# Kernel tuning notes

Hardware: AMD Instinct MI355X
Metric: run time of the kernel (lower is better)

## Reference

```python
import jax, jax.numpy as jnp
import numpy as np

B, T, D_IN, H, D2, D_OUT, N_CULT = 1024, 128, 32, 512, 256, 16, 32


def setup_inputs() -> dict:
    key = jax.random.key(0)
    ks = jax.random.split(key, 16)
    s = 0.05
    return {
        "input": jax.random.normal(ks[0], (B, T, D_IN), jnp.float32),
        "hn": jnp.zeros((1, B, H), jnp.float32),
        "cultivars": jax.random.randint(ks[1], (B, 1), 0, N_CULT, jnp.int32),
        "W1": jax.random.normal(ks[2], (D2, D_IN), jnp.float32) * s,
        "b1": jnp.zeros((D2,), jnp.float32),
        "W2": jax.random.normal(ks[3], (H, D2), jnp.float32) * s,
        "b2": jnp.zeros((H,), jnp.float32),
        "W_ih": jax.random.normal(ks[4], (3 * H, H), jnp.float32) * s,
        "W_hh": jax.random.normal(ks[5], (3 * H, H), jnp.float32) * s,
        "b_ih": jnp.zeros((3 * H,), jnp.float32),
        "b_hh": jnp.zeros((3 * H,), jnp.float32),
        "W3": jax.random.normal(ks[6], (D2, H), jnp.float32) * s,
        "b3": jnp.zeros((D2,), jnp.float32),
        "Wh": jax.random.normal(ks[7], (N_CULT, D_OUT, D2), jnp.float32) * s,
        "bh": jnp.zeros((N_CULT, D_OUT), jnp.float32),
    }


def _gru(x, h0, W_ih, W_hh, b_ih, b_hh):
    # x: [B,T,H]; h0: [B,H]. PyTorch GRU gate order: r, z, n.
    gx = jnp.einsum('bth,gh->btg', x, W_ih) + b_ih  # [B,T,3H]
    gx = jnp.swapaxes(gx, 0, 1)  # [T,B,3H]

    def step(h, gx_t):
        gh = h @ W_hh.T + b_hh
        xr, xz, xn = jnp.split(gx_t, 3, axis=-1)
        hr, hz, hnn = jnp.split(gh, 3, axis=-1)
        r = jax.nn.sigmoid(xr + hr)
        z = jax.nn.sigmoid(xz + hz)
        n = jnp.tanh(xn + r * hnn)
        h_new = (1.0 - z) * n + z * h
        return h_new, None

    h_last, _ = jax.lax.scan(step, h0, gx)
    return h_last  # [B,H]


def reference(input, hn, cultivars, W1, b1, W2, b2, W_ih, W_hh, b_ih, b_hh, W3, b3, Wh, bh):
    x = input @ W1.T + b1          # [B,T,D2]
    x = x @ W2.T + b2              # [B,T,H]
    h_last = _gru(x, hn[0], W_ih, W_hh, b_ih, b_hh)  # [B,H]
    hn_out = h_last[None]          # [1,B,H]
    out = jax.nn.relu(hn_out)
    out = jax.nn.relu(out @ W3.T + b3)[0]  # [B,D2]
    cult = cultivars[:, 0]
    # grouped per-sample head: params[i] = Wh[cult[i]] @ out[i] + bh[cult[i]]
    params = jnp.einsum('bd,bod->bo', out, Wh[cult]) + bh[cult]  # [B,D_OUT]
    return (params, hn_out)
```

## Files before the change

### kernel.cpp

```cpp
#include <hip/hip_runtime.h>


#define T_STEPS 128
#define PITCH   516
#define SLAB_ROWS 64
#define LDS_BYTES (SLAB_ROWS * PITCH * 2)

typedef __attribute__((ext_vector_type(8))) short short8;
typedef __attribute__((ext_vector_type(4))) float f32x4;
typedef __attribute__((ext_vector_type(4))) float float4v;
typedef unsigned short u16;
typedef unsigned long long u64;

static __device__ __forceinline__ u16 f2bf(float f) {
    unsigned int u = __builtin_bit_cast(unsigned int, f);
    u += 0x7FFFu + ((u >> 16) & 1u);
    return (u16)(u >> 16);
}
static __device__ __forceinline__ f32x4 mfma16(short8 a, short8 b, f32x4 c) {
    return __builtin_amdgcn_mfma_f32_16x16x32_bf16(a, b, c, 0, 0, 0);
}
static __device__ __forceinline__ void st_h16(u16* p, short8 v) {
    struct W { u64 a, b; } w = __builtin_bit_cast(W, v);
    u64* q = (u64*)p;
    __hip_atomic_store(q + 0, w.a, __ATOMIC_RELAXED, __HIP_MEMORY_SCOPE_AGENT);
    __hip_atomic_store(q + 1, w.b, __ATOMIC_RELAXED, __HIP_MEMORY_SCOPE_AGENT);
}
static __device__ __forceinline__ u64 ld_sc1_u64(const u16* p) {
    return __hip_atomic_load((const u64*)p, __ATOMIC_RELAXED, __HIP_MEMORY_SCOPE_AGENT);
}
static __device__ __forceinline__ short8 lds8(const u16* p) {
    u64 lo = *(const u64*)p;
    u64 hi = *(const u64*)(p + 4);
    struct W { u64 a, b; } w{lo, hi};
    return __builtin_bit_cast(short8, w);
}

#define WS_HBUF0 0
#define WS_HBUF1 1048576
#define WS_W21   2097152
#define WS_B21   2162688
#define WS_WEFF  2164736
#define WS_BEFF  2263040
#define WS_FLAGS 2269184

__global__ void k_prep0(const float* __restrict__ W1, const float* __restrict__ b1,
                        const float* __restrict__ W2, const float* __restrict__ b2,
                        float* __restrict__ W21, float* __restrict__ b21,
                        unsigned* __restrict__ flags) {
    if (blockIdx.x == 0) {
        __hip_atomic_store(&flags[threadIdx.x], 0u, __ATOMIC_RELAXED, __HIP_MEMORY_SCOPE_AGENT);
        __hip_atomic_store(&flags[256 + threadIdx.x], 0u, __ATOMIC_RELAXED, __HIP_MEMORY_SCOPE_AGENT);
    }
    int gid = blockIdx.x * 256 + threadIdx.x;
    int k = gid >> 5, d = gid & 31;
    float acc = 0.f;
    for (int j = 0; j < 256; ++j)
        acc += W2[k * 256 + j] * W1[j * 32 + d];
    W21[k * 32 + d] = acc;
    if (d == 0) {
        float bb = b2[k];
        for (int j = 0; j < 256; ++j) bb += W2[k * 256 + j] * b1[j];
        b21[k] = bb;
    }
}

__global__ void k_prep1(const float* __restrict__ W_ih, const float* __restrict__ b_ih,
                        const float* __restrict__ W21, const float* __restrict__ b21,
                        u16* __restrict__ Weff, float* __restrict__ beff) {
    int gid = blockIdx.x * 256 + threadIdx.x;
    int g = gid >> 5, d = gid & 31;
    float acc = 0.f;
    for (int k = 0; k < 512; ++k)
        acc += W_ih[g * 512 + k] * W21[k * 32 + d];
    Weff[g * 32 + d] = f2bf(acc);
    if (d == 0) {
        float bb = b_ih[g];
        for (int k = 0; k < 512; ++k) bb += W_ih[g * 512 + k] * b21[k];
        beff[g] = bb;
    }
}

static __device__ __forceinline__ void bar_arrive(unsigned* gflags, int slot, unsigned v) {
    __syncthreads();
    if (threadIdx.x == 0)
        __hip_atomic_store(&gflags[slot], v, __ATOMIC_RELAXED, __HIP_MEMORY_SCOPE_AGENT);
}
static __device__ __forceinline__ void bar_wait(const unsigned* gflags, unsigned v) {
    if (threadIdx.x < 64) {
        int idx = threadIdx.x & 15;
        for (;;) {
            unsigned f = __hip_atomic_load(&gflags[idx], __ATOMIC_RELAXED, __HIP_MEMORY_SCOPE_AGENT);
            if (__ballot(f >= v) == ~0ull) break;
            __builtin_amdgcn_s_sleep(1);
        }
    }
    __syncthreads();
}

__launch_bounds__(256, 1)
__global__ void k_gru(const float* __restrict__ input, const float* __restrict__ hn,
                      const float* __restrict__ W_hh, const float* __restrict__ b_hh,
                      const u16* __restrict__ Weff, const float* __restrict__ beff,
                      u16* __restrict__ hbuf0, u16* __restrict__ hbuf1,
                      unsigned* __restrict__ flags, float* __restrict__ hn_out) {
    extern __shared__ __align__(16) u16 slab[];

    const int tid  = threadIdx.x;
    const int wave = tid >> 6, lane = tid & 63;
    const int col_l = lane & 15, quad = lane >> 4;
    const int blk = blockIdx.x;
    const int grp = blk & 15, colg = blk >> 4;
    const int colbase = colg * 32;
    const int grpbase = grp * 64;
    const int wcol = wave & 1, wm = wave >> 1;
    const int cb = colbase + wcol * 16;
    unsigned* gflags = flags + grp * 32;

    {
        int b = grpbase + colg * 4 + wave;
        const float* src = hn + (size_t)b * 512 + lane * 8;
        short8 v;
        #pragma unroll
        for (int e = 0; e < 8; ++e) v[e] = (short)f2bf(src[e]);
        st_h16(hbuf0 + (size_t)b * 512 + lane * 8, v);
    }
    short8 whhf[3][16];
    #pragma unroll
    for (int g3 = 0; g3 < 3; ++g3) {
        const float* wrow = W_hh + (size_t)(g3 * 512 + cb + col_l) * 512;
        #pragma unroll
        for (int kc = 0; kc < 16; ++kc) {
            const float* p = wrow + kc * 32 + quad * 8;
            short8 v;
            #pragma unroll
            for (int e = 0; e < 8; ++e) v[e] = (short)f2bf(p[e]);
            whhf[g3][kc] = v;
        }
    }
    short8 bwx[3];
    float bx[3], bhh[3];
    #pragma unroll
    for (int g3 = 0; g3 < 3; ++g3) {
        int nr = g3 * 512 + cb + col_l;
        bwx[g3] = *(const short8*)(Weff + nr * 32 + quad * 8);
        bx[g3]  = beff[nr];
        bhh[g3] = b_hh[nr];
    }
    float hs[2][4];
    #pragma unroll
    for (int m = 0; m < 2; ++m)
        #pragma unroll
        for (int i = 0; i < 4; ++i)
            hs[m][i] = hn[(size_t)(grpbase + (wm * 2 + m) * 16 + quad * 4 + i) * 512 + cb + col_l];

    bar_arrive(gflags, colg, 1u);

    u16* bufs[2] = { hbuf0, hbuf1 };
    #pragma unroll 1
    for (int t = 0; t < T_STEPS; ++t) {
        const u16* hsrc = bufs[t & 1];
        u16* hdst = bufs[(t + 1) & 1];

        float xf[2][8];
        #pragma unroll
        for (int m = 0; m < 2; ++m) {
            const float* xp = input + (size_t)(grpbase + (wm * 2 + m) * 16 + col_l) * 4096 + t * 32 + quad * 8;
            float4v a = *(const float4v*)xp;
            float4v b = *(const float4v*)(xp + 4);
            #pragma unroll
            for (int e = 0; e < 4; ++e) { xf[m][e] = a[e]; xf[m][4 + e] = b[e]; }
        }

        bar_wait(gflags, (unsigned)(t + 1));

        {
            u64 stg[32];
            #pragma unroll
            for (int r16 = 0; r16 < 16; ++r16)
                #pragma unroll
                for (int j = 0; j < 2; ++j)
                    stg[r16 * 2 + j] = ld_sc1_u64(hsrc + (size_t)(grpbase + wave * 16 + r16) * 512 + j * 256 + lane * 4);
            #pragma unroll
            for (int r16 = 0; r16 < 16; ++r16)
                #pragma unroll
                for (int j = 0; j < 2; ++j)
                    *(u64*)&slab[(wave * 16 + r16) * PITCH + j * 256 + lane * 4] = stg[r16 * 2 + j];
        }
        __syncthreads();

        #pragma unroll
        for (int m = 0; m < 2; ++m) {
            short8 ax;
            #pragma unroll
            for (int e = 0; e < 8; ++e) ax[e] = (short)f2bf(xf[m][e]);
            f32x4 z4 = { 0.f, 0.f, 0.f, 0.f };
            f32x4 ar  = mfma16(ax, bwx[0], z4);
            f32x4 az  = mfma16(ax, bwx[1], z4);
            f32x4 anx = mfma16(ax, bwx[2], z4);
            f32x4 anh = z4;
            const int arow = ((wm * 2 + m) * 16 + col_l) * PITCH;
            #pragma unroll
            for (int kc = 0; kc < 16; ++kc) {
                short8 a = lds8(slab + arow + kc * 32 + quad * 8);
                ar  = mfma16(a, whhf[0][kc], ar);
                az  = mfma16(a, whhf[1][kc], az);
                anh = mfma16(a, whhf[2][kc], anh);
            }
            #pragma unroll
            for (int i = 0; i < 4; ++i) {
                float r = 1.f / (1.f + __expf(-(ar[i] + bx[0] + bhh[0])));
                float z = 1.f / (1.f + __expf(-(az[i] + bx[1] + bhh[1])));
                float np = anx[i] + bx[2] + r * (anh[i] + bhh[2]);
                float e  = __expf(-2.f * fabsf(np));
                float nn = __builtin_copysignf((1.f - e) / (1.f + e), np);
                float h  = (1.f - z) * nn + z * hs[m][i];
                hs[m][i] = h;
                int b = grpbase + (wm * 2 + m) * 16 + quad * 4 + i;
                __hip_atomic_store(&hdst[(size_t)b * 512 + cb + col_l], f2bf(h),
                                   __ATOMIC_RELAXED, __HIP_MEMORY_SCOPE_AGENT);
            }
        }
        bar_arrive(gflags, colg, (unsigned)(t + 2));
    }
    #pragma unroll
    for (int m = 0; m < 2; ++m)
        #pragma unroll
        for (int i = 0; i < 4; ++i)
            hn_out[(size_t)(grpbase + (wm * 2 + m) * 16 + quad * 4 + i) * 512 + cb + col_l] = hs[m][i];
}

__launch_bounds__(256)
__global__ void k_head(const u16* __restrict__ hfin, const float* __restrict__ W3,
                       const float* __restrict__ b3, const int* __restrict__ cult,
                       const float* __restrict__ Wh, const float* __restrict__ bh,
                       float* __restrict__ params) {
    __shared__ float out2[16][264];
    const int tid = threadIdx.x, wave = tid >> 6, lane = tid & 63;
    const int col_l = lane & 15, quad = lane >> 4;
    const int bbase = blockIdx.x * 16;

    f32x4 z4 = { 0.f, 0.f, 0.f, 0.f };
    f32x4 acc[4];
    #pragma unroll
    for (int nt = 0; nt < 4; ++nt) acc[nt] = z4;

    #pragma unroll
    for (int kc = 0; kc < 16; ++kc) {
        short8 a = *(const short8*)(hfin + (size_t)(bbase + col_l) * 512 + kc * 32 + quad * 8);
        #pragma unroll
        for (int e = 0; e < 8; ++e) {
            u16 v = (u16)a[e];
            a[e] = (short)((v & 0x8000u) ? 0 : v);
        }
        #pragma unroll
        for (int nt = 0; nt < 4; ++nt) {
            int nrow = wave * 64 + nt * 16 + col_l;
            const float* wr = W3 + (size_t)nrow * 512 + kc * 32 + quad * 8;
            short8 b;
            #pragma unroll
            for (int e = 0; e < 8; ++e) b[e] = (short)f2bf(wr[e]);
            acc[nt] = mfma16(a, b, acc[nt]);
        }
    }
    #pragma unroll
    for (int nt = 0; nt < 4; ++nt) {
        int ncol = wave * 64 + nt * 16 + col_l;
        float bias = b3[ncol];
        #pragma unroll
        for (int i = 0; i < 4; ++i) {
            float v = acc[nt][i] + bias;
            out2[quad * 4 + i][ncol] = v > 0.f ? v : 0.f;
        }
    }
    __syncthreads();
    int b_local = tid >> 4, o2 = tid & 15;
    int batch = bbase + b_local;
    int c = cult[batch];
    float acc2 = bh[c * 16 + o2];
    const float* wrow = Wh + (size_t)(c * 16 + o2) * 256;
    for (int d = 0; d < 256; ++d) acc2 += out2[b_local][d] * wrow[d];
    params[(size_t)batch * 16 + o2] = acc2;
}

extern "C" void kernel_launch(void* const* d_in, const int* in_sizes, int n_in,
                              void* d_out, int out_size, void* d_ws, size_t ws_size,
                              hipStream_t stream) {
    (void)in_sizes; (void)n_in; (void)out_size; (void)ws_size;
    const float* input = (const float*)d_in[0];
    const float* hn    = (const float*)d_in[1];
    const int*   cult  = (const int*)d_in[2];
    const float* W1    = (const float*)d_in[3];
    const float* b1    = (const float*)d_in[4];
    const float* W2    = (const float*)d_in[5];
    const float* b2    = (const float*)d_in[6];
    const float* W_ih  = (const float*)d_in[7];
    const float* W_hh  = (const float*)d_in[8];
    const float* b_ih  = (const float*)d_in[9];
    const float* b_hh  = (const float*)d_in[10];
    const float* W3    = (const float*)d_in[11];
    const float* b3    = (const float*)d_in[12];
    const float* Wh    = (const float*)d_in[13];
    const float* bh    = (const float*)d_in[14];

    char* ws = (char*)d_ws;
    u16*      hbuf0 = (u16*)(ws + WS_HBUF0);
    u16*      hbuf1 = (u16*)(ws + WS_HBUF1);
    float*    W21   = (float*)(ws + WS_W21);
    float*    b21   = (float*)(ws + WS_B21);
    u16*      Weff  = (u16*)(ws + WS_WEFF);
    float*    beff  = (float*)(ws + WS_BEFF);
    unsigned* flags = (unsigned*)(ws + WS_FLAGS);

    float* out    = (float*)d_out;
    float* params = out;
    float* hnout  = out + 16384;

    hipFuncSetAttribute((const void*)k_gru,
                        hipFuncAttributeMaxDynamicSharedMemorySize, LDS_BYTES);

    k_prep0<<<64, 256, 0, stream>>>(W1, b1, W2, b2, W21, b21, flags);
    k_prep1<<<192, 256, 0, stream>>>(W_ih, b_ih, W21, b21, Weff, beff);
    k_gru<<<256, 256, LDS_BYTES, stream>>>(input, hn, W_hh, b_hh, Weff, beff,
                                           hbuf0, hbuf1, flags, hnout);
    k_head<<<64, 256, 0, stream>>>(hbuf0, W3, b3, cult, Wh, bh, params);
}
```

Baseline: 809.3 us.

## Repartition GRU blocks into 32 batch groups of 8 column blocks

Changes the persistent GRU decomposition from 16 batch groups × 16 column blocks (64 rows, 32 columns each) to 32 batch groups × 8 column blocks (32 rows, 64 columns each). Each barrier now synchronizes 8 blocks instead of 16, and each block stages only 32 rows of h into a smaller static LDS slab. Row loads are staggered by column block to spread L2 traffic, and the final-step barrier arrive is skipped. Per-wave MFMA work is unchanged, but each block now needs more hidden-state columns per wave-tile and smaller groups may change L2 sharing patterns.

```diff
diff --git a/kernel.cpp b/kernel.cpp
--- a/kernel.cpp
+++ b/kernel.cpp
@@ -3,8 +3,7 @@
 
 #define T_STEPS 128
 #define PITCH   516
-#define SLAB_ROWS 64
-#define LDS_BYTES (SLAB_ROWS * PITCH * 2)
+#define SLAB_ROWS 32
 
 typedef __attribute__((ext_vector_type(8))) short short8;
 typedef __attribute__((ext_vector_type(4))) float f32x4;
@@ -48,10 +47,8 @@
                         const float* __restrict__ W2, const float* __restrict__ b2,
                         float* __restrict__ W21, float* __restrict__ b21,
                         unsigned* __restrict__ flags) {
-    if (blockIdx.x == 0) {
+    if (blockIdx.x == 0)
         __hip_atomic_store(&flags[threadIdx.x], 0u, __ATOMIC_RELAXED, __HIP_MEMORY_SCOPE_AGENT);
-        __hip_atomic_store(&flags[256 + threadIdx.x], 0u, __ATOMIC_RELAXED, __HIP_MEMORY_SCOPE_AGENT);
-    }
     int gid = blockIdx.x * 256 + threadIdx.x;
     int k = gid >> 5, d = gid & 31;
     float acc = 0.f;
@@ -88,7 +85,7 @@
 }
 static __device__ __forceinline__ void bar_wait(const unsigned* gflags, unsigned v) {
     if (threadIdx.x < 64) {
-        int idx = threadIdx.x & 15;
+        int idx = threadIdx.x & 7;
         for (;;) {
             unsigned f = __hip_atomic_load(&gflags[idx], __ATOMIC_RELAXED, __HIP_MEMORY_SCOPE_AGENT);
             if (__ballot(f >= v) == ~0ull) break;
@@ -104,18 +101,16 @@
                       const u16* __restrict__ Weff, const float* __restrict__ beff,
                       u16* __restrict__ hbuf0, u16* __restrict__ hbuf1,
                       unsigned* __restrict__ flags, float* __restrict__ hn_out) {
-    extern __shared__ __align__(16) u16 slab[];
+    __shared__ __align__(16) u16 slab[SLAB_ROWS * PITCH];
 
     const int tid  = threadIdx.x;
     const int wave = tid >> 6, lane = tid & 63;
     const int col_l = lane & 15, quad = lane >> 4;
     const int blk = blockIdx.x;
-    const int grp = blk & 15, colg = blk >> 4;
-    const int colbase = colg * 32;
-    const int grpbase = grp * 64;
-    const int wcol = wave & 1, wm = wave >> 1;
-    const int cb = colbase + wcol * 16;
-    unsigned* gflags = flags + grp * 32;
+    const int grp = blk & 31, colg = blk >> 5;
+    const int grpbase = grp * 32;
+    const int cb = colg * 64 + wave * 16;
+    unsigned* gflags = flags + grp * 8;
 
     {
         int b = grpbase + colg * 4 + wave;
@@ -152,7 +147,7 @@
     for (int m = 0; m < 2; ++m)
         #pragma unroll
         for (int i = 0; i < 4; ++i)
-            hs[m][i] = hn[(size_t)(grpbase + (wm * 2 + m) * 16 + quad * 4 + i) * 512 + cb + col_l];
+            hs[m][i] = hn[(size_t)(grpbase + m * 16 + quad * 4 + i) * 512 + cb + col_l];
 
     bar_arrive(gflags, colg, 1u);
 
@@ -165,7 +160,7 @@
         float xf[2][8];
         #pragma unroll
         for (int m = 0; m < 2; ++m) {
-            const float* xp = input + (size_t)(grpbase + (wm * 2 + m) * 16 + col_l) * 4096 + t * 32 + quad * 8;
+            const float* xp = input + (size_t)(grpbase + m * 16 + col_l) * 4096 + t * 32 + quad * 8;
             float4v a = *(const float4v*)xp;
             float4v b = *(const float4v*)(xp + 4);
             #pragma unroll
@@ -175,17 +170,21 @@
         bar_wait(gflags, (unsigned)(t + 1));
 
         {
-            u64 stg[32];
-            #pragma unroll
-            for (int r16 = 0; r16 < 16; ++r16)
+            u64 stg[16];
+            #pragma unroll
+            for (int r8 = 0; r8 < 8; ++r8) {
+                int r = (wave * 8 + r8 + colg * 4) & 31;
                 #pragma unroll
                 for (int j = 0; j < 2; ++j)
-                    stg[r16 * 2 + j] = ld_sc1_u64(hsrc + (size_t)(grpbase + wave * 16 + r16) * 512 + j * 256 + lane * 4);
-            #pragma unroll
-            for (int r16 = 0; r16 < 16; ++r16)
+                    stg[r8 * 2 + j] = ld_sc1_u64(hsrc + (size_t)(grpbase + r) * 512 + j * 256 + lane * 4);
+            }
+            #pragma unroll
+            for (int r8 = 0; r8 < 8; ++r8) {
+                int r = (wave * 8 + r8 + colg * 4) & 31;
                 #pragma unroll
                 for (int j = 0; j < 2; ++j)
-                    *(u64*)&slab[(wave * 16 + r16) * PITCH + j * 256 + lane * 4] = stg[r16 * 2 + j];
+                    *(u64*)&slab[r * PITCH + j * 256 + lane * 4] = stg[r8 * 2 + j];
+            }
         }
         __syncthreads();
 
@@ -199,7 +198,7 @@
             f32x4 az  = mfma16(ax, bwx[1], z4);
             f32x4 anx = mfma16(ax, bwx[2], z4);
             f32x4 anh = z4;
-            const int arow = ((wm * 2 + m) * 16 + col_l) * PITCH;
+            const int arow = (m * 16 + col_l) * PITCH;
             #pragma unroll
             for (int kc = 0; kc < 16; ++kc) {
                 short8 a = lds8(slab + arow + kc * 32 + quad * 8);
@@ -216,18 +215,19 @@
                 float nn = __builtin_copysignf((1.f - e) / (1.f + e), np);
                 float h  = (1.f - z) * nn + z * hs[m][i];
                 hs[m][i] = h;
-                int b = grpbase + (wm * 2 + m) * 16 + quad * 4 + i;
+                int b = grpbase + m * 16 + quad * 4 + i;
                 __hip_atomic_store(&hdst[(size_t)b * 512 + cb + col_l], f2bf(h),
                                    __ATOMIC_RELAXED, __HIP_MEMORY_SCOPE_AGENT);
             }
         }
-        bar_arrive(gflags, colg, (unsigned)(t + 2));
+        if (t < T_STEPS - 1)
+            bar_arrive(gflags, colg, (unsigned)(t + 2));
     }
     #pragma unroll
     for (int m = 0; m < 2; ++m)
         #pragma unroll
         for (int i = 0; i < 4; ++i)
-            hn_out[(size_t)(grpbase + (wm * 2 + m) * 16 + quad * 4 + i) * 512 + cb + col_l] = hs[m][i];
+            hn_out[(size_t)(grpbase + m * 16 + quad * 4 + i) * 512 + cb + col_l] = hs[m][i];
 }
 
 __launch_bounds__(256)
@@ -316,12 +316,9 @@
     float* params = out;
     float* hnout  = out + 16384;
 
-    hipFuncSetAttribute((const void*)k_gru,
-                        hipFuncAttributeMaxDynamicSharedMemorySize, LDS_BYTES);
-
     k_prep0<<<64, 256, 0, stream>>>(W1, b1, W2, b2, W21, b21, flags);
     k_prep1<<<192, 256, 0, stream>>>(W_ih, b_ih, W21, b21, Weff, beff);
-    k_gru<<<256, 256, LDS_BYTES, stream>>>(input, hn, W_hh, b_hh, Weff, beff,
-                                           hbuf0, hbuf1, flags, hnout);
+    k_gru<<<256, 256, 0, stream>>>(input, hn, W_hh, b_hh, Weff, beff,
+                                   hbuf0, hbuf1, flags, hnout);
     k_head<<<64, 256, 0, stream>>>(hbuf0, W3, b3, cult, Wh, bh, params);
 }
```

Measured after the change: 741.8 us. 8.3% less time.
